# Optimization experiments

Measured on AMD Instinct MI355X. Metric: run time of the kernel, lower is better.

The kernel has to match this reference:

```python
import jax, jax.numpy as jnp
import numpy as np

B, DH, P, V, NP, K = 8, 1024, 64, 50257, 256, 8
SKEW = P * (P - 1) // 2


def setup_inputs() -> dict:
    key = jax.random.key(0)
    ks = jax.random.split(key, 24)
    f = jax.random.normal
    h_t = f(ks[0], (B, DH), jnp.float32)
    R = f(ks[1], (B, P, P), jnp.float32)
    A_t = 0.05 * (R - jnp.swapaxes(R, -1, -2))  # skew-symmetric
    B_t = f(ks[2], (B, NP, P), jnp.float32)
    E = f(ks[3], (V, P), jnp.float32)
    e_mask = f(ks[4], (B, P), jnp.float32)
    M = f(ks[5], (B, P, P), jnp.float32)
    G_tilde = jnp.eye(P) + 0.01 * jnp.einsum('bij,bkj->bik', M, M)  # SPD metric
    z0 = f(ks[6], (B, P), jnp.float32)
    s = lambda k_, sh: f(k_, sh, jnp.float32) * 0.02
    params = dict(
        WQ_w=s(ks[7], (DH, P)), WQ_b=jnp.zeros((P,)),
        WK_w=s(ks[8], (P, P)), WK_b=jnp.zeros((P,)),
        WV_w=s(ks[9], (P, P)), WV_b=jnp.zeros((P,)),
        WC_w=s(ks[10], (P, P)), WC_b=jnp.zeros((P,)),
        WO_w=s(ks[11], (DH, V)),
        WG_w=s(ks[12], (P, P)), WG_b=jnp.zeros((P,)),
        wgamma_w=s(ks[13], (DH + P + SKEW, 1)), wgamma_b=jnp.zeros((1,)),
        wmu_w=s(ks[14], (DH + P + 2, 1)), wmu_b=jnp.zeros((1,)),
        gdown_w=s(ks[15], (SKEW, P)),
        Sigma_inv=jnp.ones((P,)) * 0.1,
        hlie_w=s(ks[16], (DH, P)), hlie_b=jnp.zeros((P,)),
    )
    return dict(h_t=h_t, A_t=A_t, B_t=B_t, E=E, e_mask=e_mask,
                G_tilde=G_tilde, z0=z0, **params)


def _sq_riem(x, Y, G):
    # x: (B,p), Y: (B,n,p), G: (B,p,p) -> (B,n)
    d = Y - x[:, None, :]
    return jnp.einsum('bnp,bpq,bnq->bn', d, G, d)


def reference(h_t, A_t, B_t, E, e_mask, G_tilde, z0,
              WQ_w, WQ_b, WK_w, WK_b, WV_w, WV_b, WC_w, WC_b, WO_w,
              WG_w, WG_b, wgamma_w, wgamma_b, wmu_w, wmu_b,
              gdown_w, Sigma_inv, hlie_w, hlie_b):
    p = A_t.shape[-1]
    scale = 1.0 / jnp.sqrt(jnp.asarray(p, h_t.dtype))
    I = jnp.eye(p, dtype=A_t.dtype)
    Q_t = jnp.linalg.solve(I - A_t, jnp.broadcast_to(I + A_t, A_t.shape))  # Cayley map (B,p,p)
    q_t = h_t @ WQ_w + WQ_b                      # (B,p)
    B_rot = jnp.einsum('bnp,bpq->bnq', B_t, Q_t)  # (B,n,p)
    K_t = B_rot @ WK_w + WK_b
    V_t = B_rot @ WV_w + WV_b
    h_lie = h_t @ hlie_w + hlie_b                 # (B,p)
    omega = -0.5 * _sq_riem(h_lie, B_rot, G_tilde)  # (B,n)
    scores = jnp.einsum('bp,bnp->bn', q_t, K_t) * scale + omega
    alpha = jax.nn.softmax(scores, axis=-1)
    c_t = jnp.einsum('bn,bnp->bp', alpha, V_t)
    iu0, iu1 = jnp.triu_indices(p, k=1)
    g_t = A_t[:, iu0, iu1]                        # (B, skew_dim)
    E_gen = E @ WG_w + WG_b                       # (V,p)
    g_proj = g_t @ gdown_w                        # (B,p)
    diff = E_gen[None, :, :] - g_proj[:, None, :]  # (B,V,p)
    kappa = -jnp.sum(diff * diff * Sigma_inv, axis=-1)  # (B,V)
    base_logits = h_t @ WO_w                      # (B,V)
    c_rot = jnp.einsum('bp,bpq->bq', c_t @ WC_w + WC_b, Q_t)
    group_logits = c_rot @ E.T * scale + kappa
    gamma = jax.nn.sigmoid(jnp.concatenate([h_t, c_t, g_t], -1) @ wgamma_w + wgamma_b)
    logits = base_logits + gamma * group_logits
    pi = jax.nn.softmax(logits, axis=-1)
    topv, topi = jax.lax.top_k(pi, K)
    topp = topv / jnp.sum(topv, -1, keepdims=True)
    E_g = E[topi]                                 # (B,k,p) gather
    E_G = jnp.einsum('bkp,bpq->bkq', E_g, Q_t)
    E_exp = jnp.einsum('bk,bkp->bp', topp, E_G)
    H = -jnp.sum(pi * jnp.log(pi + 1e-12), -1, keepdims=True)
    rho = _sq_riem(h_lie, E_exp[:, None, :], G_tilde)  # (B,1)
    mu = jax.nn.sigmoid(jnp.concatenate([h_t, c_t, H, rho], -1) @ wmu_w + wmu_b)
    m_next = mu * e_mask + (1.0 - mu) * E_exp
    outer = m_next[:, :, None] * e_mask[:, None, :]
    A_next = A_t + 0.1 * (outer - jnp.swapaxes(outer, 1, 2))
    return logits, m_next, A_next
```

## Files before the change

kernel.cpp:

```cpp
#include <hip/hip_runtime.h>
#include <math.h>

#define NV    50257
#define OUT_M 402056
#define OUT_A 402568
#define SCALE 0.125f

#define WS_Q      0
#define WS_HTR    32768
#define WS_S      40960
#define WS_TV     45056
#define WS_C0     45120
#define WS_IU     45128
#define WS_HLIE   47144
#define WS_W1     47656
#define WS_S0     48168
#define WS_GH     48176
#define WS_WMAT   48192
#define WS_SC     80960
#define WS_WB     83008
#define WS_CONSTB 83520
#define WS_GAMMA  83528
#define WS_CT     83536
#define WS_P6     84048

__global__ __launch_bounds__(256) void k1_prep(
    const float* __restrict__ h_t, const float* __restrict__ A_t,
    const float* __restrict__ WG_w, const float* __restrict__ WG_b,
    const float* __restrict__ Sigma_inv, float* __restrict__ ws)
{
    const int tid = threadIdx.x;
    const int blk = blockIdx.x;
    if (blk < 8) {
        const int b = blk;
        __shared__ float Ash[64][65];
        __shared__ float piv[2][132];
        __shared__ float fr[2][64];
        __shared__ float dsh[64];
        const int i  = tid & 63;
        const int cb = __builtin_amdgcn_readfirstlane(tid >> 6);

        for (int idx = tid; idx < 4096; idx += 256)
            Ash[idx >> 6][idx & 63] = A_t[b*4096 + idx];
        __syncthreads();

        float w[32];
        if (cb < 2) {
            #pragma unroll
            for (int jj = 0; jj < 32; ++jj) {
                int j = cb*32 + jj;
                w[jj] = (i == j ? 1.0f : 0.0f) - Ash[i][j];
            }
        } else {
            #pragma unroll
            for (int jj = 0; jj < 32; ++jj) {
                int j = (cb - 2)*32 + jj;
                w[jj] = (i == j ? 1.0f : 0.0f) + Ash[i][j];
            }
        }
        __syncthreads();

        #pragma unroll
        for (int k = 0; k < 64; ++k) {
            const int kb  = k >> 5;
            const int sel = k & 1;
            if (cb == kb) fr[sel][i] = w[k & 31];
            if (i == k) {
                #pragma unroll
                for (int q4 = 0; q4 < 8; ++q4)
                    *(float4*)&piv[sel][cb*32 + q4*4] =
                        make_float4(w[q4*4], w[q4*4+1], w[q4*4+2], w[q4*4+3]);
            }
            __syncthreads();
            float pk = piv[sel][k];
            float f = (i == k) ? 0.0f : (fr[sel][i] / pk);
            #pragma unroll
            for (int jj = 0; jj < 32; ++jj)
                w[jj] -= f * piv[sel][cb*32 + jj];
        }

        if (cb == (i >> 5)) dsh[i] = w[i & 31];
        __syncthreads();
        if (cb >= 2) {
            float dinv = 1.0f / dsh[i];
            #pragma unroll
            for (int jj = 0; jj < 32; ++jj)
                Ash[i][(cb - 2)*32 + jj] = w[jj] * dinv;
        }
        __syncthreads();
        for (int idx = tid; idx < 4096; idx += 256)
            ws[WS_Q + b*4096 + idx] = Ash[idx >> 6][idx & 63];
        for (int k = tid; k < 1024; k += 256)
            ws[WS_HTR + k*8 + b] = h_t[b*1024 + k];
    } else {
        __shared__ float Wsc[64][65];
        __shared__ float Wr[64][65];
        __shared__ float sig[64], bg[64];
        const int a  = tid & 63;
        const int cb = __builtin_amdgcn_readfirstlane(tid >> 6);
        if (tid < 64) { sig[tid] = Sigma_inv[tid]; bg[tid] = WG_b[tid]; }
        __syncthreads();
        for (int idx = tid; idx < 4096; idx += 256) {
            int r = idx >> 6, c = idx & 63;
            float wv = WG_w[idx];
            Wr[r][c] = wv; Wsc[r][c] = wv * sig[c];
        }
        __syncthreads();
        float t[16];
        #pragma unroll
        for (int j = 0; j < 16; ++j) t[j] = 0.0f;
        for (int p = 0; p < 64; ++p) {
            float wv = Wsc[a][p];
            #pragma unroll
            for (int jj = 0; jj < 16; ++jj) t[jj] += wv * Wr[cb*16 + jj][p];
        }
        #pragma unroll
        for (int jj = 0; jj < 16; ++jj)
            ws[WS_S + a*64 + cb*16 + jj] = t[jj];
        if (cb == 0) {
            float s = 0.0f;
            for (int p = 0; p < 64; ++p) s += Wsc[a][p] * bg[p];
            ws[WS_TV + a] = 2.0f * s;
        }
        if (tid == 0) {
            float c0 = 0.0f;
            for (int p = 0; p < 64; ++p) c0 += sig[p] * bg[p] * bg[p];
            ws[WS_C0] = c0;
        }
        for (int s = tid; s < 2016; s += 256) {
            int i2 = 0, f = 0;
            while (f + (63 - i2) <= s) { f += 63 - i2; ++i2; }
            int j = i2 + 1 + (s - f);
            ((int*)ws)[WS_IU + s] = i2*64 + j;
        }
    }
}

__global__ __launch_bounds__(256) void k2_batch(
    const float* __restrict__ h_t, const float* __restrict__ G_t,
    const float* __restrict__ WQ_w, const float* __restrict__ WQ_b,
    const float* __restrict__ WK_w, const float* __restrict__ WK_b,
    const float* __restrict__ wgamma_w,
    const float* __restrict__ hlie_w, const float* __restrict__ hlie_b,
    float* __restrict__ ws)
{
    __shared__ float Qsh[64][65], Gsh[64][65];
    __shared__ float hsh[1024];
    __shared__ float part[4][64], partb[4][64];
    __shared__ float qt[64], hl[64], qkv[64], ghl[64], v0[64], red64[64];
    __shared__ float scal[4];

    const int b = blockIdx.x, tid = threadIdx.x;
    const int lane = tid & 63;
    const int gu = __builtin_amdgcn_readfirstlane(tid >> 6);
    const int col0 = gu * 16;
    const float* Qb = ws + WS_Q + b*4096;
    const float* Gb = G_t + b*4096;

    for (int idx = tid; idx < 4096; idx += 256) {
        int r = idx >> 6, c = idx & 63;
        Qsh[r][c] = Qb[idx];
        Gsh[r][c] = Gb[idx];
    }
    for (int idx = tid; idx < 1024; idx += 256) hsh[idx] = h_t[b*1024 + idx];
    __syncthreads();
    {
        float aq = 0, ah = 0, ag = 0;
        #pragma unroll 8
        for (int kk = 0; kk < 256; ++kk) {
            int k = gu*256 + kk;
            float hv = hsh[k];
            aq += hv * WQ_w[k*64 + lane];
            ah += hv * hlie_w[k*64 + lane];
            ag += hv * wgamma_w[k];
        }
        part[gu][lane] = aq; partb[gu][lane] = ah;
        if (lane == 0) red64[gu] = ag;
    }
    __syncthreads();
    if (tid < 64) {
        qt[tid] = part[0][tid]+part[1][tid]+part[2][tid]+part[3][tid] + WQ_b[tid];
        hl[tid] = partb[0][tid]+partb[1][tid]+partb[2][tid]+partb[3][tid] + hlie_b[tid];
    }
    if (tid == 0) scal[0] = red64[0]+red64[1]+red64[2]+red64[3];
    __syncthreads();
    {
        float acc = 0;
        #pragma unroll
        for (int jj = 0; jj < 16; ++jj) acc += WK_w[lane*64 + col0 + jj] * qt[col0 + jj];
        part[gu][lane] = acc;
    }
    if (tid < 64) red64[tid] = qt[tid] * WK_b[tid];
    __syncthreads();
    if (tid < 64) qkv[tid] = part[0][tid]+part[1][tid]+part[2][tid]+part[3][tid];
    if (tid == 0) { float s = 0; for (int j = 0; j < 64; ++j) s += red64[j]; scal[1] = s; }
    __syncthreads();
    {
        float acc = 0;
        #pragma unroll
        for (int jj = 0; jj < 16; ++jj) acc += Gsh[lane][col0 + jj] * hl[col0 + jj];
        part[gu][lane] = acc;
    }
    __syncthreads();
    if (tid < 64) {
        float g = part[0][tid]+part[1][tid]+part[2][tid]+part[3][tid];
        ghl[tid] = g; red64[tid] = hl[tid]*g;
    }
    __syncthreads();
    if (tid == 0) { float s = 0; for (int j = 0; j < 64; ++j) s += red64[j]; scal[2] = s; }
    if (tid < 64) v0[tid] = SCALE*qkv[tid] + ghl[tid];
    __syncthreads();
    {
        float acc = 0;
        #pragma unroll
        for (int jj = 0; jj < 16; ++jj) acc += Qsh[lane][col0+jj] * v0[col0+jj];
        part[gu][lane] = acc;
    }
    __syncthreads();
    if (tid < 64) {
        ws[WS_W1 + b*64 + tid] = part[0][tid]+part[1][tid]+part[2][tid]+part[3][tid];
        ws[WS_HLIE + b*64 + tid] = hl[tid];
    }
    if (tid == 0) {
        ws[WS_S0 + b] = SCALE*scal[1] - 0.5f*scal[2];
        ws[WS_GH + b] = scal[0];
    }
    float t[16];
    #pragma unroll
    for (int j = 0; j < 16; ++j) t[j] = 0;
    for (int r = 0; r < 64; ++r) {
        float qv = Qsh[lane][r];
        #pragma unroll
        for (int j = 0; j < 16; ++j) t[j] += qv * Gsh[r][col0+j];
    }
    __syncthreads();
    #pragma unroll
    for (int j = 0; j < 16; ++j) Gsh[lane][col0+j] = t[j];
    __syncthreads();
    float w[16];
    #pragma unroll
    for (int j = 0; j < 16; ++j) w[j] = 0;
    for (int q = 0; q < 64; ++q) {
        float tv = Gsh[lane][q];
        #pragma unroll
        for (int j = 0; j < 16; ++j) w[j] += tv * Qsh[col0+j][q];
    }
    #pragma unroll
    for (int j = 0; j < 16; ++j)
        ws[WS_WMAT + b*4096 + (col0+j)*64 + lane] = w[j];
}

__global__ __launch_bounds__(256) void k3_scores(
    const float* __restrict__ B_t, float* __restrict__ ws)
{
    __shared__ float Bsh[64][65];
    __shared__ float Wsh[64][64];
    __shared__ float w1sh[64];
    __shared__ float part[4][64];
    const int b = blockIdx.x >> 2, q4 = blockIdx.x & 3;
    const int tid = threadIdx.x, lane = tid & 63;
    const int gu = __builtin_amdgcn_readfirstlane(tid >> 6);
    const int col0 = gu * 16;
    for (int idx = tid; idx < 4096; idx += 256) {
        int r = idx >> 6, c = idx & 63;
        Bsh[r][c] = B_t[b*16384 + (q4*64 + r)*64 + c];
        Wsh[r][c] = ws[WS_WMAT + b*4096 + idx];
    }
    if (tid < 64) w1sh[tid] = ws[WS_W1 + b*64 + tid];
    __syncthreads();
    float t[16];
    #pragma unroll
    for (int j = 0; j < 16; ++j) t[j] = 0;
    for (int p = 0; p < 64; ++p) {
        float bv = Bsh[lane][p];
        #pragma unroll
        for (int j = 0; j < 16; ++j) t[j] += bv * Wsh[p][col0+j];
    }
    float ps = 0;
    #pragma unroll
    for (int j = 0; j < 16; ++j) ps += (w1sh[col0+j] - 0.5f*t[j]) * Bsh[lane][col0+j];
    part[gu][lane] = ps;
    __syncthreads();
    if (tid < 64)
        ws[WS_SC + b*256 + q4*64 + tid] =
            part[0][tid]+part[1][tid]+part[2][tid]+part[3][tid] + ws[WS_S0 + b];
}

__global__ __launch_bounds__(256) void k4_mid(
    const float* __restrict__ A_t, const float* __restrict__ B_t,
    const float* __restrict__ WV_w, const float* __restrict__ WV_b,
    const float* __restrict__ WC_w, const float* __restrict__ WC_b,
    const float* __restrict__ WG_w, const float* __restrict__ WG_b,
    const float* __restrict__ wgamma_w, const float* __restrict__ wgamma_b,
    const float* __restrict__ gdown_w, const float* __restrict__ Sigma_inv,
    float* __restrict__ ws)
{
    __shared__ float alpha[256], rr[256];
    __shared__ float part[4][64];
    __shared__ float cBr[64], cB[64], ct[64], cw[64], crot[64], gp[64], uv[64];
    const int b = blockIdx.x, tid = threadIdx.x, lane = tid & 63;
    const int gu = __builtin_amdgcn_readfirstlane(tid >> 6);
    const int col0 = gu * 16;
    const float* Qb = ws + WS_Q + b*4096;

    float sv = ws[WS_SC + b*256 + tid];
    rr[tid] = sv; __syncthreads();
    for (int off = 128; off > 0; off >>= 1) { if (tid < off) rr[tid] = fmaxf(rr[tid], rr[tid+off]); __syncthreads(); }
    float smax = rr[0]; __syncthreads();
    float e = expf(sv - smax);
    rr[tid] = e; __syncthreads();
    for (int off = 128; off > 0; off >>= 1) { if (tid < off) rr[tid] += rr[tid+off]; __syncthreads(); }
    float den = rr[0]; __syncthreads();
    alpha[tid] = e / den;
    __syncthreads();
    {
        float acc = 0;
        for (int nn = 0; nn < 64; ++nn) {
            int n = gu*64 + nn;
            acc += alpha[n] * B_t[b*16384 + n*64 + lane];
        }
        part[gu][lane] = acc;
    }
    __syncthreads();
    if (tid < 64) cBr[tid] = part[0][tid]+part[1][tid]+part[2][tid]+part[3][tid];
    __syncthreads();
    {
        float acc = 0;
        #pragma unroll
        for (int pp = 0; pp < 16; ++pp) { int p = col0+pp; acc += cBr[p]*Qb[p*64+lane]; }
        part[gu][lane] = acc;
    }
    __syncthreads();
    if (tid < 64) cB[tid] = part[0][tid]+part[1][tid]+part[2][tid]+part[3][tid];
    __syncthreads();
    {
        float acc = 0;
        #pragma unroll
        for (int pp = 0; pp < 16; ++pp) { int p = col0+pp; acc += cB[p]*WV_w[p*64+lane]; }
        part[gu][lane] = acc;
    }
    __syncthreads();
    if (tid < 64) {
        float v = part[0][tid]+part[1][tid]+part[2][tid]+part[3][tid] + WV_b[tid];
        ct[tid] = v; ws[WS_CT + b*64 + tid] = v;
    }
    __syncthreads();
    {
        float acc = 0;
        #pragma unroll
        for (int pp = 0; pp < 16; ++pp) { int p = col0+pp; acc += ct[p]*WC_w[p*64+lane]; }
        part[gu][lane] = acc;
    }
    __syncthreads();
    if (tid < 64) cw[tid] = part[0][tid]+part[1][tid]+part[2][tid]+part[3][tid] + WC_b[tid];
    __syncthreads();
    {
        float acc = 0;
        #pragma unroll
        for (int pp = 0; pp < 16; ++pp) { int p = col0+pp; acc += cw[p]*Qb[p*64+lane]; }
        part[gu][lane] = acc;
    }
    __syncthreads();
    if (tid < 64) crot[tid] = part[0][tid]+part[1][tid]+part[2][tid]+part[3][tid];
    __syncthreads();
    {
        const int* iu = (const int*)ws + WS_IU;
        float accp = 0, accg = 0;
        #pragma unroll 4
        for (int ss = 0; ss < 504; ++ss) {
            int s = gu*504 + ss;
            int ij = iu[s];
            float av = A_t[b*4096 + ij];
            accp += av * gdown_w[s*64 + lane];
            accg += av * wgamma_w[1088 + s];
        }
        part[gu][lane] = accp;
        if (lane == 0) rr[gu] = accg;
    }
    if (tid < 64) rr[64 + tid] = ct[tid] * wgamma_w[1024 + tid];
    __syncthreads();
    if (tid < 64) {
        float g = part[0][tid]+part[1][tid]+part[2][tid]+part[3][tid];
        gp[tid] = g; uv[tid] = 2.0f * Sigma_inv[tid] * g;
    }
    if (tid == 0) {
        float gc = 0; for (int j = 0; j < 64; ++j) gc += rr[64 + j];
        float z = ws[WS_GH + b] + gc + rr[0]+rr[1]+rr[2]+rr[3] + wgamma_b[0];
        ws[WS_GAMMA + b] = 1.0f / (1.0f + expf(-z));
    }
    __syncthreads();
    {
        float acc = 0;
        #pragma unroll
        for (int pp = 0; pp < 16; ++pp) { int p = col0+pp; acc += WG_w[lane*64+p]*uv[p]; }
        part[gu][lane] = acc;
    }
    if (tid < 64) rr[tid] = WG_b[tid]*uv[tid] - gp[tid]*gp[tid]*Sigma_inv[tid];
    __syncthreads();
    if (tid < 64)
        ws[WS_WB + b*64 + tid] = SCALE*crot[tid]
            + part[0][tid]+part[1][tid]+part[2][tid]+part[3][tid];
    if (tid == 0) { float s = 0; for (int j = 0; j < 64; ++j) s += rr[j]; ws[WS_CONSTB + b] = s; }
}

#define KU 16
__global__ __launch_bounds__(128) void k5_logits(
    const float* __restrict__ E, const float* __restrict__ WO_w,
    const float* __restrict__ ws, float* __restrict__ out)
{
    __shared__ float smem[12608];
    const int tid = threadIdx.x;
    const int vb = blockIdx.x * 128;
    const int v = vb + tid;
    const bool vok = v < NV;
    const int vv = vok ? v : NV - 1;

    float* Esh  = smem;
    float* Ssh  = smem + 8448;
    float* tvsh = smem + 12544;
    for (int idx = tid; idx < 8192; idx += 128) {
        int r = idx >> 6, c = idx & 63;
        int vr = vb + r; if (vr >= NV) vr = NV - 1;
        Esh[r*66 + c] = E[vr*64 + c];
    }
    for (int idx = tid; idx < 4096; idx += 128) Ssh[idx] = ws[WS_S + idx];
    if (tid < 64) tvsh[tid] = ws[WS_TV + tid];
    __syncthreads();
    float sv = ws[WS_C0];
    {
        const float* er = Esh + tid*66;
        for (int jb = 0; jb < 4; ++jb) {
            float t[16];
            #pragma unroll
            for (int j = 0; j < 16; ++j) t[j] = 0;
            for (int p = 0; p < 64; ++p) {
                float ep = er[p];
                #pragma unroll
                for (int j = 0; j < 16; ++j) t[j] += ep * Ssh[p*64 + jb*16 + j];
            }
            #pragma unroll
            for (int j = 0; j < 16; ++j) sv += (t[j] + tvsh[jb*16+j]) * er[jb*16+j];
        }
    }
    __syncthreads();
    float* hsh  = smem;
    float* wbsh = smem + 8192;
    float* gmsh = smem + 8704;
    float* cbsh = smem + 8712;
    for (int idx = tid; idx < 8192; idx += 128) hsh[idx] = ws[WS_HTR + idx];
    for (int idx = tid; idx < 512; idx += 128) wbsh[idx] = ws[WS_WB + idx];
    if (tid < 8) { gmsh[tid] = ws[WS_GAMMA + tid]; cbsh[tid] = ws[WS_CONSTB + tid]; }
    __syncthreads();
    float gd[8];
    #pragma unroll
    for (int bb = 0; bb < 8; ++bb) gd[bb] = 0;
    {
        const float4* E4 = (const float4*)(E + (size_t)vv * 64);
        #pragma unroll 4
        for (int p4 = 0; p4 < 16; ++p4) {
            float4 e4 = E4[p4];
            #pragma unroll
            for (int bb = 0; bb < 8; ++bb) {
                const float* wp = wbsh + bb*64 + p4*4;
                gd[bb] += e4.x*wp[0] + e4.y*wp[1] + e4.z*wp[2] + e4.w*wp[3];
            }
        }
    }
    float acc[8];
    #pragma unroll
    for (int bb = 0; bb < 8; ++bb) acc[bb] = 0;
    {
        const float* wo = WO_w + vv;
        for (int k0 = 0; k0 < 1024; k0 += KU) {
            float wr[KU];
            #pragma unroll
            for (int u = 0; u < KU; ++u) wr[u] = wo[(size_t)(k0 + u) * NV];
            #pragma unroll
            for (int u = 0; u < KU; ++u) {
                const float* hp = hsh + (k0 + u)*8;
                #pragma unroll
                for (int bb = 0; bb < 8; ++bb) acc[bb] = fmaf(hp[bb], wr[u], acc[bb]);
            }
        }
    }
    if (vok) {
        #pragma unroll
        for (int bb = 0; bb < 8; ++bb) {
            float gl = gd[bb] + cbsh[bb] - sv;
            out[bb*NV + v] = fmaf(gmsh[bb], gl, acc[bb]);
        }
    }
}

#define NQ 12565
__global__ __launch_bounds__(256) void k6a_scan(
    const float* __restrict__ outl, float* __restrict__ ws)
{
    __shared__ float candv[2048];
    __shared__ int   candi[2048];
    __shared__ float redv[256];
    __shared__ int   redi[256];
    __shared__ int   redo[256];
    __shared__ float sred[256];
    __shared__ float t8v[8];
    __shared__ int   t8i[8];
    __shared__ int   iscal[1];
    const int b = blockIdx.x >> 2, q = blockIdx.x & 3;
    const int tid = threadIdx.x;
    const int v0 = q * NQ;
    const int v1 = (v0 + NQ < NV) ? (v0 + NQ) : NV;
    const float* lg = outl + b*NV;

    float lv[8]; int li[8];
    #pragma unroll
    for (int u = 0; u < 8; ++u) { lv[u] = -INFINITY; li[u] = 0x7fffffff; }
    for (int v = v0 + tid; v < v1; v += 256) {
        float x = lg[v];
        if (x > lv[7]) {
            int p = 7;
            while (p > 0 && x > lv[p-1]) { lv[p] = lv[p-1]; li[p] = li[p-1]; --p; }
            lv[p] = x; li[p] = v;
        }
    }
    #pragma unroll
    for (int u = 0; u < 8; ++u) { candv[tid*8 + u] = lv[u]; candi[tid*8 + u] = li[u]; }
    __syncthreads();
    int ptr = 0;
    for (int it = 0; it < 8; ++it) {
        redv[tid] = (ptr < 8) ? candv[tid*8 + ptr] : -INFINITY;
        redi[tid] = (ptr < 8) ? candi[tid*8 + ptr] : 0x7fffffff;
        redo[tid] = tid;
        __syncthreads();
        for (int off = 128; off > 0; off >>= 1) {
            if (tid < off) {
                float ov = redv[tid + off]; int oi = redi[tid + off];
                if (ov > redv[tid] || (ov == redv[tid] && oi < redi[tid])) {
                    redv[tid] = ov; redi[tid] = oi; redo[tid] = redo[tid + off];
                }
            }
            __syncthreads();
        }
        if (tid == 0) { t8v[it] = redv[0]; t8i[it] = redi[0]; iscal[0] = redo[0]; }
        __syncthreads();
        if (tid == iscal[0]) ++ptr;
        __syncthreads();
    }
    float Mp = t8v[0];
    float s1 = 0, s2 = 0;
    for (int v = v0 + tid; v < v1; v += 256) {
        float x = lg[v];
        float ee = expf(x - Mp);
        s1 += ee; s2 += x * ee;
    }
    redv[tid] = s1; sred[tid] = s2;
    __syncthreads();
    for (int off = 128; off > 0; off >>= 1) {
        if (tid < off) { redv[tid] += redv[tid+off]; sred[tid] += sred[tid+off]; }
        __syncthreads();
    }
    if (tid == 0) {
        int base = WS_P6 + (b*4 + q)*20;
        #pragma unroll
        for (int u = 0; u < 8; ++u) { ws[base + u] = t8v[u]; ((int*)ws)[base + 8 + u] = t8i[u]; }
        ws[base + 16] = Mp; ws[base + 17] = redv[0]; ws[base + 18] = sred[0];
    }
}

__global__ __launch_bounds__(256) void k6b_final(
    const float* __restrict__ h_t, const float* __restrict__ A_t,
    const float* __restrict__ E, const float* __restrict__ e_mask,
    const float* __restrict__ G_t,
    const float* __restrict__ wmu_w, const float* __restrict__ wmu_b,
    const float* __restrict__ ws, float* __restrict__ out)
{
    __shared__ float mv[32];
    __shared__ int   mi[32];
    __shared__ float t8v[8];
    __shared__ int   t8i[8];
    __shared__ float toppsh[8];
    __shared__ float redv[256];
    __shared__ float uvec[64], eexp[64], msh[64], emsh[64];
    __shared__ float scal[4];
    const int b = blockIdx.x, tid = threadIdx.x;

    if (tid < 32) {
        int base = WS_P6 + (b*4 + (tid >> 3))*20;
        mv[tid] = ws[base + (tid & 7)];
        mi[tid] = ((const int*)ws)[base + 8 + (tid & 7)];
    }
    __syncthreads();
    if (tid == 0) {
        unsigned used = 0;
        for (int it = 0; it < 8; ++it) {
            float best = -INFINITY; int bi = 0x7fffffff, bs = 0;
            for (int c = 0; c < 32; ++c) {
                if (used & (1u << c)) continue;
                float x = mv[c];
                if (x > best || (x == best && mi[c] < bi)) { best = x; bi = mi[c]; bs = c; }
            }
            used |= 1u << bs; t8v[it] = best; t8i[it] = bi;
        }
        float M = t8v[0];
        float s1 = 0, s2 = 0;
        for (int q = 0; q < 4; ++q) {
            int base = WS_P6 + (b*4 + q)*20;
            float sc_ = expf(ws[base + 16] - M);
            s1 += ws[base + 17] * sc_; s2 += ws[base + 18] * sc_;
        }
        scal[0] = M + logf(s1) - s2 / s1;
        float ts = 0, tv_[8];
        #pragma unroll
        for (int u = 0; u < 8; ++u) { tv_[u] = expf(t8v[u] - M); ts += tv_[u]; }
        #pragma unroll
        for (int u = 0; u < 8; ++u) toppsh[u] = tv_[u] / ts;
    }
    __syncthreads();
    if (tid < 64) {
        float u_ = 0;
        #pragma unroll
        for (int j = 0; j < 8; ++j) u_ += toppsh[j] * E[t8i[j]*64 + tid];
        uvec[tid] = u_;
    }
    __syncthreads();
    if (tid < 64) {
        const float* Qb = ws + WS_Q + b*4096;
        float a = 0;
        for (int p = 0; p < 64; ++p) a += uvec[p] * Qb[p*64 + tid];
        eexp[tid] = a;
    }
    __syncthreads();
    {
        const float* Gb = G_t + b*4096;
        const float* HL = ws + WS_HLIE + b*64;
        float a = 0;
        #pragma unroll 4
        for (int t2 = 0; t2 < 16; ++t2) {
            int idx = tid*16 + t2;
            int p = idx >> 6, q = idx & 63;
            a += (eexp[p] - HL[p]) * Gb[idx] * (eexp[q] - HL[q]);
        }
        redv[tid] = a;
    }
    __syncthreads();
    for (int off = 128; off > 0; off >>= 1) {
        if (tid < off) redv[tid] += redv[tid + off];
        __syncthreads();
    }
    if (tid == 0) scal[1] = redv[0];
    __syncthreads();
    float pm = 0;
    for (int k = tid; k < 1024; k += 256) pm += h_t[b*1024 + k] * wmu_w[k];
    if (tid < 64) pm += ws[WS_CT + b*64 + tid] * wmu_w[1024 + tid];
    redv[tid] = pm;
    __syncthreads();
    for (int off = 128; off > 0; off >>= 1) {
        if (tid < off) redv[tid] += redv[tid + off];
        __syncthreads();
    }
    if (tid == 0) {
        float z = redv[0] + scal[0]*wmu_w[1088] + scal[1]*wmu_w[1089] + wmu_b[0];
        scal[2] = 1.0f / (1.0f + expf(-z));
    }
    __syncthreads();
    if (tid < 64) {
        float mu = scal[2];
        float em = e_mask[b*64 + tid];
        float m = mu*em + (1.0f - mu)*eexp[tid];
        out[OUT_M + b*64 + tid] = m;
        msh[tid] = m; emsh[tid] = em;
    }
    __syncthreads();
    for (int idx = tid; idx < 4096; idx += 256) {
        int i = idx >> 6, j = idx & 63;
        out[OUT_A + b*4096 + idx] = A_t[b*4096 + idx]
            + 0.1f*(msh[i]*emsh[j] - msh[j]*emsh[i]);
    }
}

extern "C" void kernel_launch(void* const* d_in, const int* in_sizes, int n_in,
                              void* d_out, int out_size, void* d_ws, size_t ws_size,
                              hipStream_t stream)
{
    const float* h_t      = (const float*)d_in[0];
    const float* A_t      = (const float*)d_in[1];
    const float* B_t      = (const float*)d_in[2];
    const float* E        = (const float*)d_in[3];
    const float* e_mask   = (const float*)d_in[4];
    const float* G_t      = (const float*)d_in[5];
    const float* WQ_w     = (const float*)d_in[7];
    const float* WQ_b     = (const float*)d_in[8];
    const float* WK_w     = (const float*)d_in[9];
    const float* WK_b     = (const float*)d_in[10];
    const float* WV_w     = (const float*)d_in[11];
    const float* WV_b     = (const float*)d_in[12];
    const float* WC_w     = (const float*)d_in[13];
    const float* WC_b     = (const float*)d_in[14];
    const float* WO_w     = (const float*)d_in[15];
    const float* WG_w     = (const float*)d_in[16];
    const float* WG_b     = (const float*)d_in[17];
    const float* wgamma_w = (const float*)d_in[18];
    const float* wgamma_b = (const float*)d_in[19];
    const float* wmu_w    = (const float*)d_in[20];
    const float* wmu_b    = (const float*)d_in[21];
    const float* gdown_w  = (const float*)d_in[22];
    const float* Sigma_inv= (const float*)d_in[23];
    const float* hlie_w   = (const float*)d_in[24];
    const float* hlie_b   = (const float*)d_in[25];
    float* out = (float*)d_out;
    float* ws  = (float*)d_ws;

    k1_prep<<<9, 256, 0, stream>>>(h_t, A_t, WG_w, WG_b, Sigma_inv, ws);
    k2_batch<<<8, 256, 0, stream>>>(h_t, G_t, WQ_w, WQ_b, WK_w, WK_b,
                                    wgamma_w, hlie_w, hlie_b, ws);
    k3_scores<<<32, 256, 0, stream>>>(B_t, ws);
    k4_mid<<<8, 256, 0, stream>>>(A_t, B_t, WV_w, WV_b, WC_w, WC_b, WG_w, WG_b,
                                  wgamma_w, wgamma_b, gdown_w, Sigma_inv, ws);
    k5_logits<<<393, 128, 0, stream>>>(E, WO_w, ws, out);
    k6a_scan<<<32, 256, 0, stream>>>(out, ws);
    k6b_final<<<8, 256, 0, stream>>>(h_t, A_t, E, e_mask, G_t, wmu_w, wmu_b, ws, out);
}
```

Measured before the change: 593.3 us.

## Fuse prep kernels, split logits K-loop across two halves, drop per-batch score offset

Merges the Cayley-solve prep kernel with the per-batch projection kernel so one launch computes Q and the downstream vectors, removing a launch and a workspace round-trip. The logits kernel now uses 256 threads, with two halves each covering half of the 1024-long WO_w reduction and half the group-distance work, then combining through shared memory. This doubles waves per block for the memory-bound WO_w stream. k4 precomputes the upper-triangular A entries into shared memory instead of an index-table gather. The constant per-batch score offset (s0) is dropped because softmax is shift-invariant, and many accumulations are switched to fmaf.

```diff
diff --git a/kernel.cpp b/kernel.cpp
--- a/kernel.cpp
+++ b/kernel.cpp
@@ -24,158 +24,149 @@
 #define WS_CT     83536
 #define WS_P6     84048
 
-__global__ __launch_bounds__(256) void k1_prep(
+__global__ __launch_bounds__(256) void k12_prep(
     const float* __restrict__ h_t, const float* __restrict__ A_t,
+    const float* __restrict__ G_t,
     const float* __restrict__ WG_w, const float* __restrict__ WG_b,
-    const float* __restrict__ Sigma_inv, float* __restrict__ ws)
-{
-    const int tid = threadIdx.x;
-    const int blk = blockIdx.x;
-    if (blk < 8) {
-        const int b = blk;
-        __shared__ float Ash[64][65];
-        __shared__ float piv[2][132];
-        __shared__ float fr[2][64];
-        __shared__ float dsh[64];
-        const int i  = tid & 63;
-        const int cb = __builtin_amdgcn_readfirstlane(tid >> 6);
-
-        for (int idx = tid; idx < 4096; idx += 256)
-            Ash[idx >> 6][idx & 63] = A_t[b*4096 + idx];
-        __syncthreads();
-
-        float w[32];
-        if (cb < 2) {
-            #pragma unroll
-            for (int jj = 0; jj < 32; ++jj) {
-                int j = cb*32 + jj;
-                w[jj] = (i == j ? 1.0f : 0.0f) - Ash[i][j];
-            }
-        } else {
-            #pragma unroll
-            for (int jj = 0; jj < 32; ++jj) {
-                int j = (cb - 2)*32 + jj;
-                w[jj] = (i == j ? 1.0f : 0.0f) + Ash[i][j];
-            }
-        }
-        __syncthreads();
-
-        #pragma unroll
-        for (int k = 0; k < 64; ++k) {
-            const int kb  = k >> 5;
-            const int sel = k & 1;
-            if (cb == kb) fr[sel][i] = w[k & 31];
-            if (i == k) {
-                #pragma unroll
-                for (int q4 = 0; q4 < 8; ++q4)
-                    *(float4*)&piv[sel][cb*32 + q4*4] =
-                        make_float4(w[q4*4], w[q4*4+1], w[q4*4+2], w[q4*4+3]);
-            }
-            __syncthreads();
-            float pk = piv[sel][k];
-            float f = (i == k) ? 0.0f : (fr[sel][i] / pk);
-            #pragma unroll
-            for (int jj = 0; jj < 32; ++jj)
-                w[jj] -= f * piv[sel][cb*32 + jj];
-        }
-
-        if (cb == (i >> 5)) dsh[i] = w[i & 31];
-        __syncthreads();
-        if (cb >= 2) {
-            float dinv = 1.0f / dsh[i];
-            #pragma unroll
-            for (int jj = 0; jj < 32; ++jj)
-                Ash[i][(cb - 2)*32 + jj] = w[jj] * dinv;
-        }
-        __syncthreads();
-        for (int idx = tid; idx < 4096; idx += 256)
-            ws[WS_Q + b*4096 + idx] = Ash[idx >> 6][idx & 63];
-        for (int k = tid; k < 1024; k += 256)
-            ws[WS_HTR + k*8 + b] = h_t[b*1024 + k];
-    } else {
-        __shared__ float Wsc[64][65];
-        __shared__ float Wr[64][65];
-        __shared__ float sig[64], bg[64];
-        const int a  = tid & 63;
-        const int cb = __builtin_amdgcn_readfirstlane(tid >> 6);
-        if (tid < 64) { sig[tid] = Sigma_inv[tid]; bg[tid] = WG_b[tid]; }
-        __syncthreads();
-        for (int idx = tid; idx < 4096; idx += 256) {
-            int r = idx >> 6, c = idx & 63;
-            float wv = WG_w[idx];
-            Wr[r][c] = wv; Wsc[r][c] = wv * sig[c];
-        }
-        __syncthreads();
-        float t[16];
-        #pragma unroll
-        for (int j = 0; j < 16; ++j) t[j] = 0.0f;
-        for (int p = 0; p < 64; ++p) {
-            float wv = Wsc[a][p];
-            #pragma unroll
-            for (int jj = 0; jj < 16; ++jj) t[jj] += wv * Wr[cb*16 + jj][p];
-        }
-        #pragma unroll
-        for (int jj = 0; jj < 16; ++jj)
-            ws[WS_S + a*64 + cb*16 + jj] = t[jj];
-        if (cb == 0) {
-            float s = 0.0f;
-            for (int p = 0; p < 64; ++p) s += Wsc[a][p] * bg[p];
-            ws[WS_TV + a] = 2.0f * s;
-        }
-        if (tid == 0) {
-            float c0 = 0.0f;
-            for (int p = 0; p < 64; ++p) c0 += sig[p] * bg[p] * bg[p];
-            ws[WS_C0] = c0;
-        }
-        for (int s = tid; s < 2016; s += 256) {
-            int i2 = 0, f = 0;
-            while (f + (63 - i2) <= s) { f += 63 - i2; ++i2; }
-            int j = i2 + 1 + (s - f);
-            ((int*)ws)[WS_IU + s] = i2*64 + j;
-        }
-    }
-}
-
-__global__ __launch_bounds__(256) void k2_batch(
-    const float* __restrict__ h_t, const float* __restrict__ G_t,
+    const float* __restrict__ Sigma_inv,
     const float* __restrict__ WQ_w, const float* __restrict__ WQ_b,
     const float* __restrict__ WK_w, const float* __restrict__ WK_b,
     const float* __restrict__ wgamma_w,
     const float* __restrict__ hlie_w, const float* __restrict__ hlie_b,
     float* __restrict__ ws)
 {
-    __shared__ float Qsh[64][65], Gsh[64][65];
+    __shared__ float Ash[64][65];
+    __shared__ float Gsh[64][65];
     __shared__ float hsh[1024];
+    __shared__ float piv[2][132];
+    __shared__ float fr[2][64];
+    __shared__ float dsh[64];
     __shared__ float part[4][64], partb[4][64];
-    __shared__ float qt[64], hl[64], qkv[64], ghl[64], v0[64], red64[64];
-    __shared__ float scal[4];
-
-    const int b = blockIdx.x, tid = threadIdx.x;
-    const int lane = tid & 63;
-    const int gu = __builtin_amdgcn_readfirstlane(tid >> 6);
-    const int col0 = gu * 16;
-    const float* Qb = ws + WS_Q + b*4096;
-    const float* Gb = G_t + b*4096;
+    __shared__ float qt[64], hl[64], qkv[64], ghl[64], v0[64];
+    __shared__ float red64[4];
+    __shared__ float scal[1];
+
+    const int tid = threadIdx.x;
+    const int blk = blockIdx.x;
+
+    if (blk == 8) {
+        const int a   = tid & 63;
+        const int cb8 = __builtin_amdgcn_readfirstlane(tid >> 6);
+        float* sig = hsh;
+        float* bg  = hsh + 64;
+        if (tid < 64) { sig[tid] = Sigma_inv[tid]; bg[tid] = WG_b[tid]; }
+        __syncthreads();
+        for (int idx = tid; idx < 4096; idx += 256) {
+            int r = idx >> 6, c = idx & 63;
+            float wv = WG_w[idx];
+            Gsh[r][c] = wv;
+            Ash[r][c] = wv * sig[c];
+        }
+        __syncthreads();
+        float t8[16];
+        #pragma unroll
+        for (int j = 0; j < 16; ++j) t8[j] = 0.0f;
+        for (int p = 0; p < 64; ++p) {
+            float wv = Ash[a][p];
+            #pragma unroll
+            for (int jj = 0; jj < 16; ++jj) t8[jj] = fmaf(wv, Gsh[cb8*16 + jj][p], t8[jj]);
+        }
+        #pragma unroll
+        for (int jj = 0; jj < 16; ++jj)
+            ws[WS_S + a*64 + cb8*16 + jj] = t8[jj];
+        if (cb8 == 0) {
+            float s = 0.0f;
+            for (int p = 0; p < 64; ++p) s += Ash[a][p] * bg[p];
+            ws[WS_TV + a] = 2.0f * s;
+        }
+        if (tid == 0) {
+            float c0 = 0.0f;
+            for (int p = 0; p < 64; ++p) c0 += sig[p] * bg[p] * bg[p];
+            ws[WS_C0] = c0;
+        }
+        return;
+    }
+
+    const int b  = blk;
+    const int i  = tid & 63;
+    const int cb = __builtin_amdgcn_readfirstlane(tid >> 6);
+    const int col0 = cb * 16;
 
     for (int idx = tid; idx < 4096; idx += 256) {
         int r = idx >> 6, c = idx & 63;
-        Qsh[r][c] = Qb[idx];
-        Gsh[r][c] = Gb[idx];
-    }
-    for (int idx = tid; idx < 1024; idx += 256) hsh[idx] = h_t[b*1024 + idx];
-    __syncthreads();
-    {
-        float aq = 0, ah = 0, ag = 0;
+        Ash[r][c] = A_t[b*4096 + idx];
+        Gsh[r][c] = G_t[b*4096 + idx];
+    }
+    for (int k = tid; k < 1024; k += 256) {
+        float hv = h_t[b*1024 + k];
+        hsh[k] = hv;
+        ws[WS_HTR + k*8 + b] = hv;
+    }
+    __syncthreads();
+
+    float w[32];
+    if (cb < 2) {
+        #pragma unroll
+        for (int jj = 0; jj < 32; ++jj) {
+            int j = cb*32 + jj;
+            w[jj] = (i == j ? 1.0f : 0.0f) - Ash[i][j];
+        }
+    } else {
+        #pragma unroll
+        for (int jj = 0; jj < 32; ++jj) {
+            int j = (cb - 2)*32 + jj;
+            w[jj] = (i == j ? 1.0f : 0.0f) + Ash[i][j];
+        }
+    }
+    __syncthreads();
+
+    #pragma unroll
+    for (int k = 0; k < 64; ++k) {
+        const int kb  = k >> 5;
+        const int sel = k & 1;
+        if (cb == kb) fr[sel][i] = w[k & 31];
+        if (i == k) {
+            #pragma unroll
+            for (int q4 = 0; q4 < 8; ++q4)
+                *(float4*)&piv[sel][cb*32 + q4*4] =
+                    make_float4(w[q4*4], w[q4*4+1], w[q4*4+2], w[q4*4+3]);
+        }
+        __syncthreads();
+        float pk = piv[sel][k];
+        float f = (i == k) ? 0.0f : (fr[sel][i] / pk);
+        #pragma unroll
+        for (int jj = 0; jj < 32; ++jj)
+            w[jj] -= f * piv[sel][cb*32 + jj];
+    }
+
+    if (cb == (i >> 5)) dsh[i] = w[i & 31];
+    __syncthreads();
+    if (cb >= 2) {
+        float dinv = 1.0f / dsh[i];
+        #pragma unroll
+        for (int jj = 0; jj < 32; ++jj)
+            Ash[i][(cb - 2)*32 + jj] = w[jj] * dinv;
+    }
+    __syncthreads();
+    for (int idx = tid; idx < 4096; idx += 256)
+        ws[WS_Q + b*4096 + idx] = Ash[idx >> 6][idx & 63];
+
+    {
+        float aq0 = 0, aq1 = 0, ah0 = 0, ah1 = 0, ag0 = 0, ag1 = 0;
         #pragma unroll 8
-        for (int kk = 0; kk < 256; ++kk) {
-            int k = gu*256 + kk;
-            float hv = hsh[k];
-            aq += hv * WQ_w[k*64 + lane];
-            ah += hv * hlie_w[k*64 + lane];
-            ag += hv * wgamma_w[k];
-        }
-        part[gu][lane] = aq; partb[gu][lane] = ah;
-        if (lane == 0) red64[gu] = ag;
+        for (int kk = 0; kk < 256; kk += 2) {
+            int k = cb*256 + kk;
+            float hv0 = hsh[k], hv1 = hsh[k + 1];
+            aq0 = fmaf(hv0, WQ_w[k*64 + i], aq0);
+            aq1 = fmaf(hv1, WQ_w[(k+1)*64 + i], aq1);
+            ah0 = fmaf(hv0, hlie_w[k*64 + i], ah0);
+            ah1 = fmaf(hv1, hlie_w[(k+1)*64 + i], ah1);
+            ag0 = fmaf(hv0, wgamma_w[k], ag0);
+            ag1 = fmaf(hv1, wgamma_w[k+1], ag1);
+        }
+        part[cb][i] = aq0 + aq1;
+        partb[cb][i] = ah0 + ah1;
+        if (i == 0) red64[cb] = ag0 + ag1;
     }
     __syncthreads();
     if (tid < 64) {
@@ -187,67 +178,62 @@
     {
         float acc = 0;
         #pragma unroll
-        for (int jj = 0; jj < 16; ++jj) acc += WK_w[lane*64 + col0 + jj] * qt[col0 + jj];
-        part[gu][lane] = acc;
-    }
-    if (tid < 64) red64[tid] = qt[tid] * WK_b[tid];
+        for (int jj = 0; jj < 16; ++jj)
+            acc = fmaf(WK_w[i*64 + col0 + jj], qt[col0 + jj], acc);
+        part[cb][i] = acc;
+    }
     __syncthreads();
     if (tid < 64) qkv[tid] = part[0][tid]+part[1][tid]+part[2][tid]+part[3][tid];
-    if (tid == 0) { float s = 0; for (int j = 0; j < 64; ++j) s += red64[j]; scal[1] = s; }
-    __syncthreads();
-    {
-        float acc = 0;
-        #pragma unroll
-        for (int jj = 0; jj < 16; ++jj) acc += Gsh[lane][col0 + jj] * hl[col0 + jj];
-        part[gu][lane] = acc;
+    __syncthreads();
+    {
+        float acc = 0;
+        #pragma unroll
+        for (int jj = 0; jj < 16; ++jj)
+            acc = fmaf(Gsh[i][col0 + jj], hl[col0 + jj], acc);
+        part[cb][i] = acc;
     }
     __syncthreads();
     if (tid < 64) {
-        float g = part[0][tid]+part[1][tid]+part[2][tid]+part[3][tid];
-        ghl[tid] = g; red64[tid] = hl[tid]*g;
-    }
-    __syncthreads();
-    if (tid == 0) { float s = 0; for (int j = 0; j < 64; ++j) s += red64[j]; scal[2] = s; }
-    if (tid < 64) v0[tid] = SCALE*qkv[tid] + ghl[tid];
-    __syncthreads();
-    {
-        float acc = 0;
-        #pragma unroll
-        for (int jj = 0; jj < 16; ++jj) acc += Qsh[lane][col0+jj] * v0[col0+jj];
-        part[gu][lane] = acc;
+        ghl[tid] = part[0][tid]+part[1][tid]+part[2][tid]+part[3][tid];
+        v0[tid]  = SCALE*qkv[tid] + ghl[tid];
+    }
+    __syncthreads();
+    {
+        float acc = 0;
+        #pragma unroll
+        for (int jj = 0; jj < 16; ++jj)
+            acc = fmaf(Ash[i][col0 + jj], v0[col0 + jj], acc);
+        part[cb][i] = acc;
     }
     __syncthreads();
     if (tid < 64) {
-        ws[WS_W1 + b*64 + tid] = part[0][tid]+part[1][tid]+part[2][tid]+part[3][tid];
+        ws[WS_W1 + b*64 + tid]   = part[0][tid]+part[1][tid]+part[2][tid]+part[3][tid];
         ws[WS_HLIE + b*64 + tid] = hl[tid];
     }
-    if (tid == 0) {
-        ws[WS_S0 + b] = SCALE*scal[1] - 0.5f*scal[2];
-        ws[WS_GH + b] = scal[0];
-    }
+    if (tid == 0) ws[WS_GH + b] = scal[0];
     float t[16];
     #pragma unroll
     for (int j = 0; j < 16; ++j) t[j] = 0;
     for (int r = 0; r < 64; ++r) {
-        float qv = Qsh[lane][r];
-        #pragma unroll
-        for (int j = 0; j < 16; ++j) t[j] += qv * Gsh[r][col0+j];
-    }
-    __syncthreads();
-    #pragma unroll
-    for (int j = 0; j < 16; ++j) Gsh[lane][col0+j] = t[j];
-    __syncthreads();
-    float w[16];
-    #pragma unroll
-    for (int j = 0; j < 16; ++j) w[j] = 0;
+        float qv = Ash[i][r];
+        #pragma unroll
+        for (int j = 0; j < 16; ++j) t[j] = fmaf(qv, Gsh[r][col0 + j], t[j]);
+    }
+    __syncthreads();
+    #pragma unroll
+    for (int j = 0; j < 16; ++j) Gsh[i][col0 + j] = t[j];
+    __syncthreads();
+    float w2r[16];
+    #pragma unroll
+    for (int j = 0; j < 16; ++j) w2r[j] = 0;
     for (int q = 0; q < 64; ++q) {
-        float tv = Gsh[lane][q];
-        #pragma unroll
-        for (int j = 0; j < 16; ++j) w[j] += tv * Qsh[col0+j][q];
+        float tv = Gsh[i][q];
+        #pragma unroll
+        for (int j = 0; j < 16; ++j) w2r[j] = fmaf(tv, Ash[col0 + j][q], w2r[j]);
     }
     #pragma unroll
     for (int j = 0; j < 16; ++j)
-        ws[WS_WMAT + b*4096 + (col0+j)*64 + lane] = w[j];
+        ws[WS_WMAT + b*4096 + (col0 + j)*64 + i] = w2r[j];
 }
 
 __global__ __launch_bounds__(256) void k3_scores(
@@ -274,7 +260,7 @@
     for (int p = 0; p < 64; ++p) {
         float bv = Bsh[lane][p];
         #pragma unroll
-        for (int j = 0; j < 16; ++j) t[j] += bv * Wsh[p][col0+j];
+        for (int j = 0; j < 16; ++j) t[j] = fmaf(bv, Wsh[p][col0 + j], t[j]);
     }
     float ps = 0;
     #pragma unroll
@@ -283,7 +269,7 @@
     __syncthreads();
     if (tid < 64)
         ws[WS_SC + b*256 + q4*64 + tid] =
-            part[0][tid]+part[1][tid]+part[2][tid]+part[3][tid] + ws[WS_S0 + b];
+            part[0][tid]+part[1][tid]+part[2][tid]+part[3][tid];
 }
 
 __global__ __launch_bounds__(256) void k4_mid(
@@ -298,11 +284,19 @@
     __shared__ float alpha[256], rr[256];
     __shared__ float part[4][64];
     __shared__ float cBr[64], cB[64], ct[64], cw[64], crot[64], gp[64], uv[64];
+    __shared__ float gsh[2016];
     const int b = blockIdx.x, tid = threadIdx.x, lane = tid & 63;
     const int gu = __builtin_amdgcn_readfirstlane(tid >> 6);
     const int col0 = gu * 16;
     const float* Qb = ws + WS_Q + b*4096;
 
+    for (int idx = tid; idx < 4096; idx += 256) {
+        int i2 = idx >> 6, j2 = idx & 63;
+        if (j2 > i2) {
+            int s = i2*63 - ((i2*(i2-1)) >> 1) + (j2 - i2 - 1);
+            gsh[s] = A_t[b*4096 + idx];
+        }
+    }
     float sv = ws[WS_SC + b*256 + tid];
     rr[tid] = sv; __syncthreads();
     for (int off = 128; off > 0; off >>= 1) { if (tid < off) rr[tid] = fmaxf(rr[tid], rr[tid+off]); __syncthreads(); }
@@ -317,7 +311,7 @@
         float acc = 0;
         for (int nn = 0; nn < 64; ++nn) {
             int n = gu*64 + nn;
-            acc += alpha[n] * B_t[b*16384 + n*64 + lane];
+            acc = fmaf(alpha[n], B_t[b*16384 + n*64 + lane], acc);
         }
         part[gu][lane] = acc;
     }
@@ -327,7 +321,7 @@
     {
         float acc = 0;
         #pragma unroll
-        for (int pp = 0; pp < 16; ++pp) { int p = col0+pp; acc += cBr[p]*Qb[p*64+lane]; }
+        for (int pp = 0; pp < 16; ++pp) { int p = col0+pp; acc = fmaf(cBr[p], Qb[p*64+lane], acc); }
         part[gu][lane] = acc;
     }
     __syncthreads();
@@ -336,7 +330,7 @@
     {
         float acc = 0;
         #pragma unroll
-        for (int pp = 0; pp < 16; ++pp) { int p = col0+pp; acc += cB[p]*WV_w[p*64+lane]; }
+        for (int pp = 0; pp < 16; ++pp) { int p = col0+pp; acc = fmaf(cB[p], WV_w[p*64+lane], acc); }
         part[gu][lane] = acc;
     }
     __syncthreads();
@@ -348,7 +342,7 @@
     {
         float acc = 0;
         #pragma unroll
-        for (int pp = 0; pp < 16; ++pp) { int p = col0+pp; acc += ct[p]*WC_w[p*64+lane]; }
+        for (int pp = 0; pp < 16; ++pp) { int p = col0+pp; acc = fmaf(ct[p], WC_w[p*64+lane], acc); }
         part[gu][lane] = acc;
     }
     __syncthreads();
@@ -357,25 +351,25 @@
     {
         float acc = 0;
         #pragma unroll
-        for (int pp = 0; pp < 16; ++pp) { int p = col0+pp; acc += cw[p]*Qb[p*64+lane]; }
+        for (int pp = 0; pp < 16; ++pp) { int p = col0+pp; acc = fmaf(cw[p], Qb[p*64+lane], acc); }
         part[gu][lane] = acc;
     }
     __syncthreads();
     if (tid < 64) crot[tid] = part[0][tid]+part[1][tid]+part[2][tid]+part[3][tid];
     __syncthreads();
     {
-        const int* iu = (const int*)ws + WS_IU;
-        float accp = 0, accg = 0;
+        float accp0 = 0, accp1 = 0, accg0 = 0, accg1 = 0;
         #pragma unroll 4
-        for (int ss = 0; ss < 504; ++ss) {
+        for (int ss = 0; ss < 504; ss += 2) {
             int s = gu*504 + ss;
-            int ij = iu[s];
-            float av = A_t[b*4096 + ij];
-            accp += av * gdown_w[s*64 + lane];
-            accg += av * wgamma_w[1088 + s];
-        }
-        part[gu][lane] = accp;
-        if (lane == 0) rr[gu] = accg;
+            float av0 = gsh[s], av1 = gsh[s + 1];
+            accp0 = fmaf(av0, gdown_w[s*64 + lane], accp0);
+            accp1 = fmaf(av1, gdown_w[(s+1)*64 + lane], accp1);
+            accg0 = fmaf(av0, wgamma_w[1088 + s], accg0);
+            accg1 = fmaf(av1, wgamma_w[1089 + s], accg1);
+        }
+        part[gu][lane] = accp0 + accp1;
+        if (lane == 0) rr[gu] = accg0 + accg1;
     }
     if (tid < 64) rr[64 + tid] = ct[tid] * wgamma_w[1024 + tid];
     __syncthreads();
@@ -392,7 +386,7 @@
     {
         float acc = 0;
         #pragma unroll
-        for (int pp = 0; pp < 16; ++pp) { int p = col0+pp; acc += WG_w[lane*64+p]*uv[p]; }
+        for (int pp = 0; pp < 16; ++pp) { int p = col0+pp; acc = fmaf(WG_w[lane*64+p], uv[p], acc); }
         part[gu][lane] = acc;
     }
     if (tid < 64) rr[tid] = WG_b[tid]*uv[tid] - gp[tid]*gp[tid]*Sigma_inv[tid];
@@ -404,90 +398,111 @@
 }
 
 #define KU 16
-__global__ __launch_bounds__(128) void k5_logits(
+__global__ __launch_bounds__(256) void k5_logits(
     const float* __restrict__ E, const float* __restrict__ WO_w,
     const float* __restrict__ ws, float* __restrict__ out)
 {
-    __shared__ float smem[12608];
-    const int tid = threadIdx.x;
+    __shared__ float smem[14544];
+    const int tid  = threadIdx.x;
+    const int half = tid >> 7;
+    const int vt   = tid & 127;
     const int vb = blockIdx.x * 128;
-    const int v = vb + tid;
+    const int v = vb + vt;
     const bool vok = v < NV;
     const int vv = vok ? v : NV - 1;
 
     float* Esh  = smem;
     float* Ssh  = smem + 8448;
     float* tvsh = smem + 12544;
-    for (int idx = tid; idx < 8192; idx += 128) {
-        int r = idx >> 6, c = idx & 63;
+    float* wbsh = smem + 12608;
+    float* gmsh = smem + 13120;
+    float* cbsh = smem + 13128;
+    float* svsh = smem + 13136;
+    float* gdsh = smem + 13392;
+
+    for (int idx = tid; idx < 2048; idx += 256) {
+        int r = idx >> 4, c4 = (idx & 15) * 4;
         int vr = vb + r; if (vr >= NV) vr = NV - 1;
-        Esh[r*66 + c] = E[vr*64 + c];
-    }
-    for (int idx = tid; idx < 4096; idx += 128) Ssh[idx] = ws[WS_S + idx];
+        float4 e4 = *(const float4*)(E + (size_t)vr * 64 + c4);
+        float* dst = Esh + r*66 + c4;
+        dst[0] = e4.x; dst[1] = e4.y; dst[2] = e4.z; dst[3] = e4.w;
+    }
+    for (int idx = tid; idx < 4096; idx += 256) Ssh[idx] = ws[WS_S + idx];
+    for (int idx = tid; idx < 512; idx += 256) wbsh[idx] = ws[WS_WB + idx];
     if (tid < 64) tvsh[tid] = ws[WS_TV + tid];
-    __syncthreads();
-    float sv = ws[WS_C0];
-    {
-        const float* er = Esh + tid*66;
-        for (int jb = 0; jb < 4; ++jb) {
+    if (tid < 8) { gmsh[tid] = ws[WS_GAMMA + tid]; cbsh[tid] = ws[WS_CONSTB + tid]; }
+    __syncthreads();
+    {
+        const float* er = Esh + vt*66;
+        float sv = (half == 0) ? ws[WS_C0] : 0.0f;
+        #pragma unroll
+        for (int jj = 0; jj < 2; ++jj) {
+            const int jb = half*2 + jj;
             float t[16];
             #pragma unroll
-            for (int j = 0; j < 16; ++j) t[j] = 0;
+            for (int j = 0; j < 16; ++j) t[j] = 0.0f;
             for (int p = 0; p < 64; ++p) {
                 float ep = er[p];
                 #pragma unroll
-                for (int j = 0; j < 16; ++j) t[j] += ep * Ssh[p*64 + jb*16 + j];
+                for (int j = 0; j < 16; ++j)
+                    t[j] = fmaf(ep, Ssh[p*64 + jb*16 + j], t[j]);
             }
             #pragma unroll
-            for (int j = 0; j < 16; ++j) sv += (t[j] + tvsh[jb*16+j]) * er[jb*16+j];
-        }
-    }
-    __syncthreads();
-    float* hsh  = smem;
-    float* wbsh = smem + 8192;
-    float* gmsh = smem + 8704;
-    float* cbsh = smem + 8712;
-    for (int idx = tid; idx < 8192; idx += 128) hsh[idx] = ws[WS_HTR + idx];
-    for (int idx = tid; idx < 512; idx += 128) wbsh[idx] = ws[WS_WB + idx];
-    if (tid < 8) { gmsh[tid] = ws[WS_GAMMA + tid]; cbsh[tid] = ws[WS_CONSTB + tid]; }
-    __syncthreads();
-    float gd[8];
-    #pragma unroll
-    for (int bb = 0; bb < 8; ++bb) gd[bb] = 0;
-    {
-        const float4* E4 = (const float4*)(E + (size_t)vv * 64);
-        #pragma unroll 4
-        for (int p4 = 0; p4 < 16; ++p4) {
-            float4 e4 = E4[p4];
-            #pragma unroll
-            for (int bb = 0; bb < 8; ++bb) {
-                const float* wp = wbsh + bb*64 + p4*4;
-                gd[bb] += e4.x*wp[0] + e4.y*wp[1] + e4.z*wp[2] + e4.w*wp[3];
-            }
-        }
-    }
+            for (int j = 0; j < 16; ++j)
+                sv += (t[j] + tvsh[jb*16 + j]) * er[jb*16 + j];
+        }
+        svsh[half*128 + vt] = sv;
+        const float* w0 = wbsh + (half*4    )*64;
+        const float* w1 = wbsh + (half*4 + 1)*64;
+        const float* w2 = wbsh + (half*4 + 2)*64;
+        const float* w3 = wbsh + (half*4 + 3)*64;
+        float g0 = 0, g1 = 0, g2 = 0, g3 = 0;
+        #pragma unroll 8
+        for (int p = 0; p < 64; ++p) {
+            float ep = er[p];
+            g0 = fmaf(ep, w0[p], g0); g1 = fmaf(ep, w1[p], g1);
+            g2 = fmaf(ep, w2[p], g2); g3 = fmaf(ep, w3[p], g3);
+        }
+        float* gr = gdsh + vt*9 + half*4;
+        gr[0] = g0; gr[1] = g1; gr[2] = g2; gr[3] = g3;
+    }
+    __syncthreads();
+    float* hsh   = smem;
+    float* accsh = smem + 8192;
+    for (int idx = tid; idx < 8192; idx += 256) hsh[idx] = ws[WS_HTR + idx];
+    __syncthreads();
     float acc[8];
     #pragma unroll
-    for (int bb = 0; bb < 8; ++bb) acc[bb] = 0;
-    {
-        const float* wo = WO_w + vv;
-        for (int k0 = 0; k0 < 1024; k0 += KU) {
+    for (int bb = 0; bb < 8; ++bb) acc[bb] = 0.0f;
+    {
+        const float* wo = WO_w + (size_t)(half * 512) * NV + vv;
+        const float* hb = hsh + half*512*8;
+        for (int k0 = 0; k0 < 512; k0 += KU) {
             float wr[KU];
             #pragma unroll
             for (int u = 0; u < KU; ++u) wr[u] = wo[(size_t)(k0 + u) * NV];
             #pragma unroll
             for (int u = 0; u < KU; ++u) {
-                const float* hp = hsh + (k0 + u)*8;
+                const float* hp = hb + (k0 + u)*8;
                 #pragma unroll
                 for (int bb = 0; bb < 8; ++bb) acc[bb] = fmaf(hp[bb], wr[u], acc[bb]);
             }
         }
     }
-    if (vok) {
+    if (half == 1) {
+        float* ar = accsh + vt*9;
+        #pragma unroll
+        for (int bb = 0; bb < 8; ++bb) ar[bb] = acc[bb];
+    }
+    __syncthreads();
+    if (half == 0 && vok) {
+        const float* ar = accsh + vt*9;
+        const float* gr = gdsh + vt*9;
+        float svt = svsh[vt] + svsh[128 + vt];
         #pragma unroll
         for (int bb = 0; bb < 8; ++bb) {
-            float gl = gd[bb] + cbsh[bb] - sv;
-            out[bb*NV + v] = fmaf(gmsh[bb], gl, acc[bb]);
+            float gl = gr[bb] + cbsh[bb] - svt;
+            out[bb*NV + v] = fmaf(gmsh[bb], gl, acc[bb] + ar[bb]);
         }
     }
 }
@@ -709,13 +724,13 @@
     float* out = (float*)d_out;
     float* ws  = (float*)d_ws;
 
-    k1_prep<<<9, 256, 0, stream>>>(h_t, A_t, WG_w, WG_b, Sigma_inv, ws);
-    k2_batch<<<8, 256, 0, stream>>>(h_t, G_t, WQ_w, WQ_b, WK_w, WK_b,
-                                    wgamma_w, hlie_w, hlie_b, ws);
+    k12_prep<<<9, 256, 0, stream>>>(h_t, A_t, G_t, WG_w, WG_b, Sigma_inv,
+                                    WQ_w, WQ_b, WK_w, WK_b, wgamma_w,
+                                    hlie_w, hlie_b, ws);
     k3_scores<<<32, 256, 0, stream>>>(B_t, ws);
     k4_mid<<<8, 256, 0, stream>>>(A_t, B_t, WV_w, WV_b, WC_w, WC_b, WG_w, WG_b,
                                   wgamma_w, wgamma_b, gdown_w, Sigma_inv, ws);
-    k5_logits<<<393, 128, 0, stream>>>(E, WO_w, ws, out);
+    k5_logits<<<393, 256, 0, stream>>>(E, WO_w, ws, out);
     k6a_scan<<<32, 256, 0, stream>>>(out, ws);
     k6b_final<<<8, 256, 0, stream>>>(h_t, A_t, E, e_mask, G_t, wmu_w, wmu_b, ws, out);
 }
```

Result: faster. 551.0 us (-7.1%).
